# Performance work log

Hardware: AMD Instinct MI355X
Metric: run time of the kernel (lower is better)

## Reference

```python
import jax, jax.numpy as jnp
import numpy as np

N_NODES = 100000
N_EDGES = 640000
D_IN = 128
D_HID = 128
D_OUT = 128


def setup_inputs() -> dict:
    key = jax.random.key(0)
    k1, k2, k3, k4 = jax.random.split(key, 4)
    x = jax.random.normal(k1, (N_NODES, D_IN), dtype=jnp.float32)
    edge_index = jax.random.randint(k2, (2, N_EDGES), 0, N_NODES, dtype=jnp.int64)
    # Linear weights (PyTorch Linear: y = x @ W.T + b; we store W as [in, out])
    W1 = jax.random.normal(k3, (D_IN, D_HID), dtype=jnp.float32) * (1.0 / np.sqrt(D_IN))
    b1 = jnp.zeros((D_HID,), dtype=jnp.float32)
    W2 = jax.random.normal(k4, (D_HID, D_OUT), dtype=jnp.float32) * (1.0 / np.sqrt(D_HID))
    b2 = jnp.zeros((D_OUT,), dtype=jnp.float32)
    return {"x": x, "edge_index": edge_index, "W1": W1, "b1": b1, "W2": W2, "b2": b2}


def _gin_conv(x, src, dst, W, b):
    # sum_{j in N(i)} x_j  (message from src to dst), PyG GINConv with eps=0:
    # out = nn((1+eps)*x + aggr)
    agg = jax.ops.segment_sum(x[src], dst, num_segments=N_NODES)
    return (x + agg) @ W + b


def reference(x, edge_index, W1, b1, W2, b2):
    src, dst = edge_index[0], edge_index[1]
    h = jax.nn.relu(_gin_conv(x, src, dst, W1, b1))
    out = _gin_conv(h, src, dst, W2, b2)
    return out
```

## Files before the change

### kernel.cpp

```cpp
#include <hip/hip_runtime.h>

#define NODES 100000
#define EDGES 640000
#define DF 128
#define SLOT 24
#define OVF_CAP 4096
#define MBLK 1563

typedef short bf16x8 __attribute__((ext_vector_type(8)));
typedef float f32x4 __attribute__((ext_vector_type(4)));

__device__ __forceinline__ unsigned short f2bf(float f) {
    unsigned u = __builtin_bit_cast(unsigned, f);
    u += 0x7FFFu + ((u >> 16) & 1u);
    return (unsigned short)(u >> 16);
}
__device__ __forceinline__ float bflo(unsigned w) { return __builtin_bit_cast(float, w << 16); }
__device__ __forceinline__ float bfhi(unsigned w) { return __builtin_bit_cast(float, w & 0xFFFF0000u); }

__global__ void prep_all(const float* __restrict__ W1, const float* __restrict__ W2,
                         unsigned short* __restrict__ Wt1, unsigned short* __restrict__ Wt2,
                         uint4* __restrict__ cursor4, int* __restrict__ ovf) {
    const int idx = blockIdx.x * blockDim.x + threadIdx.x;
    if (idx < 32768) {
        const float* src = (idx < 16384) ? W1 : W2;
        unsigned short* dst = (idx < 16384) ? Wt1 : Wt2;
        const int r = idx & 16383;
        const int n = r & 127, k = r >> 7;
        dst[n * 128 + k] = f2bf(src[k * 128 + n]);
    } else {
        const int z = idx - 32768;
        if (z < NODES / 4) cursor4[z] = make_uint4(0u, 0u, 0u, 0u);
        else if (z == NODES / 4) ovf[0] = 0;
    }
}

__global__ void fill_bucket(const int* __restrict__ srcIdx,
                            const int* __restrict__ dstIdx,
                            int* __restrict__ cursor,
                            int* __restrict__ slots,
                            int* __restrict__ ovf) {
    const int e = blockIdx.x * blockDim.x + threadIdx.x;
    if (e < EDGES) {
        const int d = dstIdx[e];
        const int s = srcIdx[e];
        const int pos = atomicAdd(&cursor[d], 1);
        if (pos < SLOT) {
            slots[d * SLOT + pos] = s;
        } else {
            const int k = atomicAdd(&ovf[0], 1);
            if (k < OVF_CAP) { ovf[1 + 2 * k] = d; ovf[2 + 2 * k] = s; }
        }
    }
}

template <int A_F32>
__global__ __launch_bounds__(256) void gemm_mfma(const void* __restrict__ Ap,
                                                 const uint4* __restrict__ Wt4,
                                                 unsigned short* __restrict__ outh) {
    __shared__ __align__(16) unsigned char wlds[32768];
    __shared__ __align__(16) unsigned char epi[16384];

    const int tid = threadIdx.x;
    #pragma unroll
    for (int i = 0; i < 8; ++i) {
        const int c = i * 256 + tid;
        const uint4 v = Wt4[c];
        const int byte = (c * 16) ^ (((c >> 4) & 7) << 4);
        *(uint4*)(wlds + byte) = v;
    }

    const int wv = tid >> 6;
    const int l  = tid & 63;
    const int lr = l & 15;
    const int g  = l >> 4;
    const int row0 = blockIdx.x * 64 + wv * 16;

    int arow = row0 + lr;
    if (arow >= NODES) arow = 0;

    bf16x8 af[4];
    if constexpr (A_F32) {
        const float* Af = (const float*)Ap + (size_t)arow * DF + g * 8;
        #pragma unroll
        for (int t = 0; t < 4; ++t) {
            const float4 f0 = *(const float4*)(Af + t * 32);
            const float4 f1 = *(const float4*)(Af + t * 32 + 4);
            bf16x8 v;
            v[0] = (short)f2bf(f0.x); v[1] = (short)f2bf(f0.y);
            v[2] = (short)f2bf(f0.z); v[3] = (short)f2bf(f0.w);
            v[4] = (short)f2bf(f1.x); v[5] = (short)f2bf(f1.y);
            v[6] = (short)f2bf(f1.z); v[7] = (short)f2bf(f1.w);
            af[t] = v;
        }
    } else {
        const unsigned short* Ab = (const unsigned short*)Ap + (size_t)arow * DF + g * 8;
        #pragma unroll
        for (int t = 0; t < 4; ++t) af[t] = *(const bf16x8*)(Ab + t * 32);
    }

    f32x4 acc[8];
    #pragma unroll
    for (int nt = 0; nt < 8; ++nt) acc[nt] = (f32x4)(0.f);

    __syncthreads();

    #pragma unroll
    for (int t = 0; t < 4; ++t) {
        #pragma unroll
        for (int nt = 0; nt < 8; ++nt) {
            const int byte = ((nt * 16 + lr) * 256 + ((((t * 4 + g) * 16) ^ ((l & 7) << 4))));
            const bf16x8 bf = *(const bf16x8*)(wlds + byte);
            acc[nt] = __builtin_amdgcn_mfma_f32_16x16x32_bf16(af[t], bf, acc[nt], 0, 0, 0);
        }
    }

    unsigned char* my = epi + wv * 4096;
    #pragma unroll
    for (int nt = 0; nt < 8; ++nt) {
        #pragma unroll
        for (int r = 0; r < 4; ++r) {
            const int R = g * 4 + r;
            const int byte = (R * 256 + (nt * 16 + lr) * 2) ^ ((R & 7) << 4);
            *(unsigned short*)(my + byte) = f2bf(acc[nt][r]);
        }
    }
    __syncthreads();
    #pragma unroll
    for (int p = 0; p < 4; ++p) {
        const int R = p * 4 + g;
        const uint4 v = *(const uint4*)(my + ((R * 256 + lr * 16) ^ ((R & 7) << 4)));
        const int gr = row0 + R;
        if (gr < NODES) *(uint4*)(outh + (size_t)gr * DF + lr * 8) = v;
    }
}

template <int RELU, int OUT_F32>
__global__ __launch_bounds__(256) void gather_bias(const uint4* __restrict__ yb,
                                                   const int* __restrict__ cursor,
                                                   const int* __restrict__ slots,
                                                   const int* __restrict__ ovf,
                                                   const float* __restrict__ bias,
                                                   void* __restrict__ outp) {
    const int gid = blockIdx.x * 256 + threadIdx.x;
    const int node = gid >> 4;
    const int lane = gid & 15;
    if (node >= NODES) return;

    float a[8];
    {
        const uint4 u = yb[(size_t)node * 16 + lane];
        a[0] = bflo(u.x); a[1] = bfhi(u.x);
        a[2] = bflo(u.y); a[3] = bfhi(u.y);
        a[4] = bflo(u.z); a[5] = bfhi(u.z);
        a[6] = bflo(u.w); a[7] = bfhi(u.w);
    }
    const int deg = min(cursor[node], SLOT);
    const int base = node * SLOT;
    int j = 0;
    for (; j + 4 <= deg; j += 4) {
        const int s0 = slots[base + j + 0];
        const int s1 = slots[base + j + 1];
        const int s2 = slots[base + j + 2];
        const int s3 = slots[base + j + 3];
        const uint4 v0 = yb[(size_t)s0 * 16 + lane];
        const uint4 v1 = yb[(size_t)s1 * 16 + lane];
        const uint4 v2 = yb[(size_t)s2 * 16 + lane];
        const uint4 v3 = yb[(size_t)s3 * 16 + lane];
        a[0] += bflo(v0.x); a[1] += bfhi(v0.x); a[2] += bflo(v0.y); a[3] += bfhi(v0.y);
        a[4] += bflo(v0.z); a[5] += bfhi(v0.z); a[6] += bflo(v0.w); a[7] += bfhi(v0.w);
        a[0] += bflo(v1.x); a[1] += bfhi(v1.x); a[2] += bflo(v1.y); a[3] += bfhi(v1.y);
        a[4] += bflo(v1.z); a[5] += bfhi(v1.z); a[6] += bflo(v1.w); a[7] += bfhi(v1.w);
        a[0] += bflo(v2.x); a[1] += bfhi(v2.x); a[2] += bflo(v2.y); a[3] += bfhi(v2.y);
        a[4] += bflo(v2.z); a[5] += bfhi(v2.z); a[6] += bflo(v2.w); a[7] += bfhi(v2.w);
        a[0] += bflo(v3.x); a[1] += bfhi(v3.x); a[2] += bflo(v3.y); a[3] += bfhi(v3.y);
        a[4] += bflo(v3.z); a[5] += bfhi(v3.z); a[6] += bflo(v3.w); a[7] += bfhi(v3.w);
    }
    for (; j < deg; ++j) {
        const uint4 v = yb[(size_t)slots[base + j] * 16 + lane];
        a[0] += bflo(v.x); a[1] += bfhi(v.x); a[2] += bflo(v.y); a[3] += bfhi(v.y);
        a[4] += bflo(v.z); a[5] += bfhi(v.z); a[6] += bflo(v.w); a[7] += bfhi(v.w);
    }

    const int oc = ovf[0];
    if (oc > 0) {
        const int m = min(oc, OVF_CAP);
        for (int k = 0; k < m; ++k) {
            if (ovf[1 + 2 * k] == node) {
                const uint4 v = yb[(size_t)ovf[2 + 2 * k] * 16 + lane];
                a[0] += bflo(v.x); a[1] += bfhi(v.x); a[2] += bflo(v.y); a[3] += bfhi(v.y);
                a[4] += bflo(v.z); a[5] += bfhi(v.z); a[6] += bflo(v.w); a[7] += bfhi(v.w);
            }
        }
    }

    const float4 bb0 = ((const float4*)bias)[lane * 2 + 0];
    const float4 bb1 = ((const float4*)bias)[lane * 2 + 1];
    a[0] += bb0.x; a[1] += bb0.y; a[2] += bb0.z; a[3] += bb0.w;
    a[4] += bb1.x; a[5] += bb1.y; a[6] += bb1.z; a[7] += bb1.w;
    if (RELU) {
        #pragma unroll
        for (int e = 0; e < 8; ++e) a[e] = fmaxf(a[e], 0.f);
    }

    if constexpr (OUT_F32) {
        float* of = (float*)outp + (size_t)node * DF + lane * 8;
        *(float4*)(of + 0) = make_float4(a[0], a[1], a[2], a[3]);
        *(float4*)(of + 4) = make_float4(a[4], a[5], a[6], a[7]);
    } else {
        uint4 o;
        o.x = (unsigned)f2bf(a[0]) | ((unsigned)f2bf(a[1]) << 16);
        o.y = (unsigned)f2bf(a[2]) | ((unsigned)f2bf(a[3]) << 16);
        o.z = (unsigned)f2bf(a[4]) | ((unsigned)f2bf(a[5]) << 16);
        o.w = (unsigned)f2bf(a[6]) | ((unsigned)f2bf(a[7]) << 16);
        ((uint4*)outp)[(size_t)node * 16 + lane] = o;
    }
}

extern "C" void kernel_launch(void* const* d_in, const int* in_sizes, int n_in,
                              void* d_out, int out_size, void* d_ws, size_t ws_size,
                              hipStream_t stream) {
    const float* x  = (const float*)d_in[0];
    const int*   ei = (const int*)d_in[1];
    const float* W1 = (const float*)d_in[2];
    const float* b1 = (const float*)d_in[3];
    const float* W2 = (const float*)d_in[4];
    const float* b2 = (const float*)d_in[5];
    float* out = (float*)d_out;

    const int* src = ei;
    const int* dst = ei + EDGES;

    unsigned short* B0  = (unsigned short*)d_ws;
    unsigned short* B1  = B0 + (size_t)NODES * DF;
    unsigned short* Wt1 = B1 + (size_t)NODES * DF;
    unsigned short* Wt2 = Wt1 + 16384;
    int* cursor = (int*)(Wt2 + 16384);
    int* slots  = cursor + NODES;
    int* ovf    = slots + (size_t)NODES * SLOT;

    prep_all<<<(32768 + NODES / 4 + 1 + 255) / 256, 256, 0, stream>>>(W1, W2, Wt1, Wt2,
                                                                      (uint4*)cursor, ovf);
    fill_bucket<<<(EDGES + 255) / 256, 256, 0, stream>>>(src, dst, cursor, slots, ovf);

    const int gblocks = (NODES * 16 + 255) / 256;

    gemm_mfma<1><<<MBLK, 256, 0, stream>>>((const void*)x, (const uint4*)Wt1, B0);
    gather_bias<1, 0><<<gblocks, 256, 0, stream>>>((const uint4*)B0, cursor, slots, ovf, b1, B1);
    gemm_mfma<0><<<MBLK, 256, 0, stream>>>((const void*)B1, (const uint4*)Wt2, B0);
    gather_bias<0, 1><<<gblocks, 256, 0, stream>>>((const uint4*)B0, cursor, slots, ovf, b2, out);
}
```

Baseline: 146.3 us.

## Replace global per-node atomic bucketing with two-pass coarse scatter and LDS fill

Replaces the single edge-bucketing kernel, which did a global atomicAdd per edge on per-node cursors, with two passes. The first scatters edges into 8x1024 coarse cells of 98 nodes each, with cell counters spread by block index. The second builds per-node slot lists in shared memory, one workgroup per node range, and writes them out coalesced. This trades scattered global atomics and writes for an extra kernel launch and an intermediate buffer. Coarse cells are capped at 128 entries and spill to the overflow list, which could overflow its own cap.

```diff
diff --git a/kernel.cpp b/kernel.cpp
--- a/kernel.cpp
+++ b/kernel.cpp
@@ -6,6 +6,9 @@
 #define SLOT 24
 #define OVF_CAP 4096
 #define MBLK 1563
+#define NB 1024
+#define NPB 98
+#define CAP 128
 
 typedef short bf16x8 __attribute__((ext_vector_type(8)));
 typedef float f32x4 __attribute__((ext_vector_type(4)));
@@ -20,7 +23,7 @@
 
 __global__ void prep_all(const float* __restrict__ W1, const float* __restrict__ W2,
                          unsigned short* __restrict__ Wt1, unsigned short* __restrict__ Wt2,
-                         uint4* __restrict__ cursor4, int* __restrict__ ovf) {
+                         uint4* __restrict__ cbc4, int* __restrict__ ovf) {
     const int idx = blockIdx.x * blockDim.x + threadIdx.x;
     if (idx < 32768) {
         const float* src = (idx < 16384) ? W1 : W2;
@@ -30,27 +33,67 @@
         dst[n * 128 + k] = f2bf(src[k * 128 + n]);
     } else {
         const int z = idx - 32768;
-        if (z < NODES / 4) cursor4[z] = make_uint4(0u, 0u, 0u, 0u);
-        else if (z == NODES / 4) ovf[0] = 0;
-    }
-}
-
-__global__ void fill_bucket(const int* __restrict__ srcIdx,
-                            const int* __restrict__ dstIdx,
-                            int* __restrict__ cursor,
-                            int* __restrict__ slots,
-                            int* __restrict__ ovf) {
-    const int e = blockIdx.x * blockDim.x + threadIdx.x;
-    if (e < EDGES) {
-        const int d = dstIdx[e];
-        const int s = srcIdx[e];
-        const int pos = atomicAdd(&cursor[d], 1);
-        if (pos < SLOT) {
-            slots[d * SLOT + pos] = s;
-        } else {
-            const int k = atomicAdd(&ovf[0], 1);
-            if (k < OVF_CAP) { ovf[1 + 2 * k] = d; ovf[2 + 2 * k] = s; }
-        }
+        if (z < (8 * NB) / 4) cbc4[z] = make_uint4(0u, 0u, 0u, 0u);
+        else if (z == (8 * NB) / 4) ovf[0] = 0;
+    }
+}
+
+__global__ void scatter_coarse(const int* __restrict__ srcIdx,
+                               const int* __restrict__ dstIdx,
+                               int* __restrict__ cbc,
+                               int2* __restrict__ coarse,
+                               int* __restrict__ ovf) {
+    const int e = blockIdx.x * 256 + threadIdx.x;
+    if (e >= EDGES) return;
+    const int d = dstIdx[e];
+    const int s = srcIdx[e];
+    const int cell = (blockIdx.x & 7) * NB + d / NPB;
+    const int pos = atomicAdd(&cbc[cell], 1);
+    if (pos < CAP) {
+        coarse[(size_t)cell * CAP + pos] = make_int2(s, d);
+    } else {
+        const int k = atomicAdd(&ovf[0], 1);
+        if (k < OVF_CAP) { ovf[1 + 2 * k] = d; ovf[2 + 2 * k] = s; }
+    }
+}
+
+__global__ __launch_bounds__(256) void bucket_fill(const int* __restrict__ cbc,
+                                                   const int2* __restrict__ coarse,
+                                                   int* __restrict__ cursor,
+                                                   int* __restrict__ slots,
+                                                   int* __restrict__ ovf) {
+    __shared__ int lcur[NPB];
+    __shared__ int lslot[NPB * SLOT];
+    const int b = blockIdx.x;
+    const int tid = threadIdx.x;
+    if (tid < NPB) lcur[tid] = 0;
+    __syncthreads();
+
+    #pragma unroll
+    for (int x = 0; x < 8; ++x) {
+        const int cell = x * NB + b;
+        const int cnt = min(cbc[cell], CAP);
+        for (int i = tid; i < cnt; i += 256) {
+            const int2 ed = coarse[(size_t)cell * CAP + i];
+            const int ln = ed.y - b * NPB;
+            const int pos = atomicAdd(&lcur[ln], 1);
+            if (pos < SLOT) {
+                lslot[ln * SLOT + pos] = ed.x;
+            } else {
+                const int k = atomicAdd(&ovf[0], 1);
+                if (k < OVF_CAP) { ovf[1 + 2 * k] = ed.y; ovf[2 + 2 * k] = ed.x; }
+            }
+        }
+    }
+    __syncthreads();
+
+    if (tid < NPB) {
+        const int g = b * NPB + tid;
+        if (g < NODES) cursor[g] = lcur[tid];
+    }
+    for (int i = tid; i < NPB * SLOT; i += 256) {
+        const int g = b * NPB + i / SLOT;
+        if (g < NODES) slots[(size_t)b * NPB * SLOT + i] = lslot[i];
     }
 }
 
@@ -237,11 +280,14 @@
     unsigned short* Wt2 = Wt1 + 16384;
     int* cursor = (int*)(Wt2 + 16384);
     int* slots  = cursor + NODES;
-    int* ovf    = slots + (size_t)NODES * SLOT;
-
-    prep_all<<<(32768 + NODES / 4 + 1 + 255) / 256, 256, 0, stream>>>(W1, W2, Wt1, Wt2,
-                                                                      (uint4*)cursor, ovf);
-    fill_bucket<<<(EDGES + 255) / 256, 256, 0, stream>>>(src, dst, cursor, slots, ovf);
+    int* cbc    = slots + (size_t)NODES * SLOT;
+    int* ovf    = cbc + 8 * NB;
+    int2* coarse = (int2*)(((size_t)(ovf + 1 + 2 * OVF_CAP) + 15) & ~(size_t)15);
+
+    prep_all<<<(32768 + 8 * NB / 4 + 1 + 255) / 256, 256, 0, stream>>>(W1, W2, Wt1, Wt2,
+                                                                       (uint4*)cbc, ovf);
+    scatter_coarse<<<(EDGES + 255) / 256, 256, 0, stream>>>(src, dst, cbc, coarse, ovf);
+    bucket_fill<<<NB, 256, 0, stream>>>(cbc, coarse, cursor, slots, ovf);
 
     const int gblocks = (NODES * 16 + 255) / 256;
 
```

Measured after the change: 148.2 us. About the same (+1.3%).

## Fuse edge bucketing into first GEMM launch as independent block range

Applied to the files above, without the earlier changes.

Merges the edge bucket-fill kernel and the first layer's feature GEMM into one launch. Blocks below FILLBLK do the atomic bucketing and the rest do the GEMM, so the two independent jobs run concurrently and one launch is removed. The fused GEMM also drops LDS staging of the weights and reads B fragments straight from global memory. That saves the LDS fill and the sync before the MFMA loop, but adds global/L2 traffic and latency inside it.

```diff
diff --git a/kernel.cpp b/kernel.cpp
--- a/kernel.cpp
+++ b/kernel.cpp
@@ -6,6 +6,7 @@
 #define SLOT 24
 #define OVF_CAP 4096
 #define MBLK 1563
+#define FILLBLK 2500
 
 typedef short bf16x8 __attribute__((ext_vector_type(8)));
 typedef float f32x4 __attribute__((ext_vector_type(4)));
@@ -35,53 +36,46 @@
     }
 }
 
-__global__ void fill_bucket(const int* __restrict__ srcIdx,
-                            const int* __restrict__ dstIdx,
-                            int* __restrict__ cursor,
-                            int* __restrict__ slots,
-                            int* __restrict__ ovf) {
-    const int e = blockIdx.x * blockDim.x + threadIdx.x;
-    if (e < EDGES) {
-        const int d = dstIdx[e];
-        const int s = srcIdx[e];
-        const int pos = atomicAdd(&cursor[d], 1);
-        if (pos < SLOT) {
-            slots[d * SLOT + pos] = s;
-        } else {
-            const int k = atomicAdd(&ovf[0], 1);
-            if (k < OVF_CAP) { ovf[1 + 2 * k] = d; ovf[2 + 2 * k] = s; }
-        }
-    }
-}
-
-template <int A_F32>
-__global__ __launch_bounds__(256) void gemm_mfma(const void* __restrict__ Ap,
-                                                 const uint4* __restrict__ Wt4,
-                                                 unsigned short* __restrict__ outh) {
-    __shared__ __align__(16) unsigned char wlds[32768];
+__global__ __launch_bounds__(256) void fill_gemm(const float* __restrict__ x,
+                                                 const unsigned short* __restrict__ Wt,
+                                                 unsigned short* __restrict__ outh,
+                                                 const int* __restrict__ srcIdx,
+                                                 const int* __restrict__ dstIdx,
+                                                 int* __restrict__ cursor,
+                                                 int* __restrict__ slots,
+                                                 int* __restrict__ ovf) {
     __shared__ __align__(16) unsigned char epi[16384];
 
+    if (blockIdx.x < FILLBLK) {
+        const int e = blockIdx.x * 256 + threadIdx.x;
+        if (e < EDGES) {
+            const int d = dstIdx[e];
+            const int s = srcIdx[e];
+            const int pos = atomicAdd(&cursor[d], 1);
+            if (pos < SLOT) {
+                slots[d * SLOT + pos] = s;
+            } else {
+                const int k = atomicAdd(&ovf[0], 1);
+                if (k < OVF_CAP) { ovf[1 + 2 * k] = d; ovf[2 + 2 * k] = s; }
+            }
+        }
+        return;
+    }
+
+    const int gb = blockIdx.x - FILLBLK;
     const int tid = threadIdx.x;
-    #pragma unroll
-    for (int i = 0; i < 8; ++i) {
-        const int c = i * 256 + tid;
-        const uint4 v = Wt4[c];
-        const int byte = (c * 16) ^ (((c >> 4) & 7) << 4);
-        *(uint4*)(wlds + byte) = v;
-    }
-
     const int wv = tid >> 6;
     const int l  = tid & 63;
     const int lr = l & 15;
     const int g  = l >> 4;
-    const int row0 = blockIdx.x * 64 + wv * 16;
+    const int row0 = gb * 64 + wv * 16;
 
     int arow = row0 + lr;
     if (arow >= NODES) arow = 0;
 
     bf16x8 af[4];
-    if constexpr (A_F32) {
-        const float* Af = (const float*)Ap + (size_t)arow * DF + g * 8;
+    {
+        const float* Af = x + (size_t)arow * DF + g * 8;
         #pragma unroll
         for (int t = 0; t < 4; ++t) {
             const float4 f0 = *(const float4*)(Af + t * 32);
@@ -93,10 +87,70 @@
             v[6] = (short)f2bf(f1.z); v[7] = (short)f2bf(f1.w);
             af[t] = v;
         }
-    } else {
-        const unsigned short* Ab = (const unsigned short*)Ap + (size_t)arow * DF + g * 8;
-        #pragma unroll
-        for (int t = 0; t < 4; ++t) af[t] = *(const bf16x8*)(Ab + t * 32);
+    }
+
+    f32x4 acc[8];
+    #pragma unroll
+    for (int nt = 0; nt < 8; ++nt) acc[nt] = (f32x4)(0.f);
+
+    #pragma unroll
+    for (int t = 0; t < 4; ++t) {
+        #pragma unroll
+        for (int nt = 0; nt < 8; ++nt) {
+            const bf16x8 bf = *(const bf16x8*)(Wt + (nt * 16 + lr) * DF + t * 32 + g * 8);
+            acc[nt] = __builtin_amdgcn_mfma_f32_16x16x32_bf16(af[t], bf, acc[nt], 0, 0, 0);
+        }
+    }
+
+    unsigned char* my = epi + wv * 4096;
+    #pragma unroll
+    for (int nt = 0; nt < 8; ++nt) {
+        #pragma unroll
+        for (int r = 0; r < 4; ++r) {
+            const int R = g * 4 + r;
+            const int byte = (R * 256 + (nt * 16 + lr) * 2) ^ ((R & 7) << 4);
+            *(unsigned short*)(my + byte) = f2bf(acc[nt][r]);
+        }
+    }
+    __syncthreads();
+    #pragma unroll
+    for (int p = 0; p < 4; ++p) {
+        const int R = p * 4 + g;
+        const uint4 v = *(const uint4*)(my + ((R * 256 + lr * 16) ^ ((R & 7) << 4)));
+        const int gr = row0 + R;
+        if (gr < NODES) *(uint4*)(outh + (size_t)gr * DF + lr * 8) = v;
+    }
+}
+
+__global__ __launch_bounds__(256) void gemm_mfma(const unsigned short* __restrict__ Ab,
+                                                 const uint4* __restrict__ Wt4,
+                                                 unsigned short* __restrict__ outh) {
+    __shared__ __align__(16) unsigned char wlds[32768];
+    __shared__ __align__(16) unsigned char epi[16384];
+
+    const int tid = threadIdx.x;
+    #pragma unroll
+    for (int i = 0; i < 8; ++i) {
+        const int c = i * 256 + tid;
+        const uint4 v = Wt4[c];
+        const int byte = (c * 16) ^ (((c >> 4) & 7) << 4);
+        *(uint4*)(wlds + byte) = v;
+    }
+
+    const int wv = tid >> 6;
+    const int l  = tid & 63;
+    const int lr = l & 15;
+    const int g  = l >> 4;
+    const int row0 = blockIdx.x * 64 + wv * 16;
+
+    int arow = row0 + lr;
+    if (arow >= NODES) arow = 0;
+
+    bf16x8 af[4];
+    {
+        const unsigned short* Ar = Ab + (size_t)arow * DF + g * 8;
+        #pragma unroll
+        for (int t = 0; t < 4; ++t) af[t] = *(const bf16x8*)(Ar + t * 32);
     }
 
     f32x4 acc[8];
@@ -241,12 +295,10 @@
 
     prep_all<<<(32768 + NODES / 4 + 1 + 255) / 256, 256, 0, stream>>>(W1, W2, Wt1, Wt2,
                                                                       (uint4*)cursor, ovf);
-    fill_bucket<<<(EDGES + 255) / 256, 256, 0, stream>>>(src, dst, cursor, slots, ovf);
-
     const int gblocks = (NODES * 16 + 255) / 256;
 
-    gemm_mfma<1><<<MBLK, 256, 0, stream>>>((const void*)x, (const uint4*)Wt1, B0);
+    fill_gemm<<<FILLBLK + MBLK, 256, 0, stream>>>(x, Wt1, B0, src, dst, cursor, slots, ovf);
     gather_bias<1, 0><<<gblocks, 256, 0, stream>>>((const uint4*)B0, cursor, slots, ovf, b1, B1);
-    gemm_mfma<0><<<MBLK, 256, 0, stream>>>((const void*)B1, (const uint4*)Wt2, B0);
+    gemm_mfma<<<MBLK, 256, 0, stream>>>(B1, (const uint4*)Wt2, B0);
     gather_bias<0, 1><<<gblocks, 256, 0, stream>>>((const uint4*)B0, cursor, slots, ovf, b2, out);
 }
```

Result: slower. 161.9 us (+10.7%).

## Build per-node edge slots via two-pass LDS binning instead of global atomics

Applied to the files above, without the earlier changes.

Replaces the single-pass edge bucketing, which did one global atomicAdd per edge on a per-node cursor, with two kernels. The first bins edges into 100 coarse destination ranges using shared-memory counters and writes them out grouped by bin. The second has one block per bin build the per-node slot lists in LDS and write them back coalesced. This cuts scattered global atomics and random writes, but adds an extra kernel launch, an intermediate buffer, and bin-build kernels that run on only 100 blocks with large LDS use, limiting parallelism.

```diff
diff --git a/kernel.cpp b/kernel.cpp
--- a/kernel.cpp
+++ b/kernel.cpp
@@ -7,6 +7,13 @@
 #define OVF_CAP 4096
 #define MBLK 1563
 
+#define BINS 100
+#define NPB 1000
+#define CAP1 96
+#define GCAP 8000
+#define CHUNK 4000
+#define P1BLK 160
+
 typedef short bf16x8 __attribute__((ext_vector_type(8)));
 typedef float f32x4 __attribute__((ext_vector_type(4)));
 
@@ -20,7 +27,7 @@
 
 __global__ void prep_all(const float* __restrict__ W1, const float* __restrict__ W2,
                          unsigned short* __restrict__ Wt1, unsigned short* __restrict__ Wt2,
-                         uint4* __restrict__ cursor4, int* __restrict__ ovf) {
+                         int* __restrict__ gcnt, int* __restrict__ ovf) {
     const int idx = blockIdx.x * blockDim.x + threadIdx.x;
     if (idx < 32768) {
         const float* src = (idx < 16384) ? W1 : W2;
@@ -30,28 +37,99 @@
         dst[n * 128 + k] = f2bf(src[k * 128 + n]);
     } else {
         const int z = idx - 32768;
-        if (z < NODES / 4) cursor4[z] = make_uint4(0u, 0u, 0u, 0u);
-        else if (z == NODES / 4) ovf[0] = 0;
-    }
-}
-
-__global__ void fill_bucket(const int* __restrict__ srcIdx,
-                            const int* __restrict__ dstIdx,
-                            int* __restrict__ cursor,
-                            int* __restrict__ slots,
-                            int* __restrict__ ovf) {
-    const int e = blockIdx.x * blockDim.x + threadIdx.x;
-    if (e < EDGES) {
+        if (z < BINS) gcnt[z] = 0;
+        else if (z == BINS) ovf[0] = 0;
+    }
+}
+
+__global__ __launch_bounds__(256) void bin_scatter(const int* __restrict__ srcIdx,
+                                                   const int* __restrict__ dstIdx,
+                                                   int* __restrict__ gcnt,
+                                                   int2* __restrict__ gbin,
+                                                   int* __restrict__ ovf) {
+    __shared__ int2 lsbin[BINS * CAP1];
+    __shared__ int lcnt[BINS];
+    __shared__ int lbase[BINS];
+    __shared__ int pref[BINS + 1];
+
+    const int tid = threadIdx.x;
+    for (int i = tid; i < BINS; i += 256) lcnt[i] = 0;
+    __syncthreads();
+
+    const int e0 = blockIdx.x * CHUNK;
+    for (int i = tid; i < CHUNK; i += 256) {
+        const int e = e0 + i;
         const int d = dstIdx[e];
         const int s = srcIdx[e];
-        const int pos = atomicAdd(&cursor[d], 1);
-        if (pos < SLOT) {
-            slots[d * SLOT + pos] = s;
+        const int b = d / NPB;
+        const int pos = atomicAdd(&lcnt[b], 1);
+        if (pos < CAP1) {
+            lsbin[b * CAP1 + pos] = make_int2(s, d);
         } else {
             const int k = atomicAdd(&ovf[0], 1);
             if (k < OVF_CAP) { ovf[1 + 2 * k] = d; ovf[2 + 2 * k] = s; }
         }
     }
+    __syncthreads();
+
+    if (tid < BINS) {
+        const int c = min(lcnt[tid], CAP1);
+        lcnt[tid] = c;
+        lbase[tid] = atomicAdd(&gcnt[tid], c);
+    }
+    __syncthreads();
+    if (tid == 0) {
+        int acc = 0;
+        for (int b = 0; b < BINS; ++b) { pref[b] = acc; acc += lcnt[b]; }
+        pref[BINS] = acc;
+    }
+    __syncthreads();
+
+    const int total = pref[BINS];
+    for (int f = tid; f < total; f += 256) {
+        int lo = 0, hi = BINS - 1;
+        while (lo < hi) { const int mid = (lo + hi + 1) >> 1; if (pref[mid] <= f) lo = mid; else hi = mid - 1; }
+        const int j = f - pref[lo];
+        const int gi = lbase[lo] + j;
+        const int2 ed = lsbin[lo * CAP1 + j];
+        if (gi < GCAP) {
+            gbin[(size_t)lo * GCAP + gi] = ed;
+        } else {
+            const int k = atomicAdd(&ovf[0], 1);
+            if (k < OVF_CAP) { ovf[1 + 2 * k] = ed.y; ovf[2 + 2 * k] = ed.x; }
+        }
+    }
+}
+
+__global__ __launch_bounds__(256) void bin_build(const int* __restrict__ gcnt,
+                                                 const int2* __restrict__ gbin,
+                                                 int* __restrict__ cursor,
+                                                 int* __restrict__ slots,
+                                                 int* __restrict__ ovf) {
+    __shared__ int lcur[NPB];
+    __shared__ int lslot[NPB * SLOT];
+    const int b = blockIdx.x;
+    const int tid = threadIdx.x;
+    for (int i = tid; i < NPB; i += 256) lcur[i] = 0;
+    __syncthreads();
+
+    const int cnt = min(gcnt[b], GCAP);
+    for (int i = tid; i < cnt; i += 256) {
+        const int2 ed = gbin[(size_t)b * GCAP + i];
+        const int ln = ed.y - b * NPB;
+        const int pos = atomicAdd(&lcur[ln], 1);
+        if (pos < SLOT) {
+            lslot[ln * SLOT + pos] = ed.x;
+        } else {
+            const int k = atomicAdd(&ovf[0], 1);
+            if (k < OVF_CAP) { ovf[1 + 2 * k] = ed.y; ovf[2 + 2 * k] = ed.x; }
+        }
+    }
+    __syncthreads();
+
+    for (int i = tid; i < NPB; i += 256) cursor[b * NPB + i] = lcur[i];
+    for (int i = tid; i < NPB * SLOT; i += 256)
+        slots[(size_t)b * NPB * SLOT + i] = lslot[i];
 }
 
 template <int A_F32>
@@ -237,11 +315,13 @@
     unsigned short* Wt2 = Wt1 + 16384;
     int* cursor = (int*)(Wt2 + 16384);
     int* slots  = cursor + NODES;
-    int* ovf    = slots + (size_t)NODES * SLOT;
-
-    prep_all<<<(32768 + NODES / 4 + 1 + 255) / 256, 256, 0, stream>>>(W1, W2, Wt1, Wt2,
-                                                                      (uint4*)cursor, ovf);
-    fill_bucket<<<(EDGES + 255) / 256, 256, 0, stream>>>(src, dst, cursor, slots, ovf);
+    int* gcnt   = slots + (size_t)NODES * SLOT;
+    int* ovf    = gcnt + BINS;
+    int2* gbin  = (int2*)(((size_t)(ovf + 1 + 2 * OVF_CAP) + 15) & ~(size_t)15);
+
+    prep_all<<<(32768 + BINS + 1 + 255) / 256, 256, 0, stream>>>(W1, W2, Wt1, Wt2, gcnt, ovf);
+    bin_scatter<<<P1BLK, 256, 0, stream>>>(src, dst, gcnt, gbin, ovf);
+    bin_build<<<BINS, 256, 0, stream>>>(gcnt, gbin, cursor, slots, ovf);
 
     const int gblocks = (NODES * 16 + 255) / 256;
 
```

Result: faster. 140.3 us (-4.1%).
